# Performance work log

Hardware: AMD Instinct MI355X
Metric: run time of the kernel (lower is better)

The kernel has to match this reference:

```python
import jax, jax.numpy as jnp
import numpy as np

HEADS = 16
NEG_INF = -1e30


def rel_shift(t):
    # t: [b, h, i, j] with i == j; Transformer-XL style relative shift
    b, h, i, j = t.shape
    t = jnp.pad(t, ((0, 0), (0, 0), (0, 0), (1, 0)))  # zero pad on last dim front
    t = t.reshape(b, h, j + 1, i)[:, :, 1:]
    return t.reshape(b, h, i, j)


def setup_inputs() -> dict:
    key = jax.random.key(0)
    ks = jax.random.split(key, 8)
    b, n, dim = 2, 2048, 1024
    d_head = dim // HEADS
    w = 0.02
    return {
        "x": jax.random.normal(ks[0], (b, n, dim), dtype=jnp.float32),
        "pos_emb": jax.random.normal(ks[1], (n, dim), dtype=jnp.float32),
        "Wq": jax.random.normal(ks[2], (dim, dim), dtype=jnp.float32) * w,
        "bq": jnp.zeros((dim,), dtype=jnp.float32),
        "Wkv": jax.random.normal(ks[3], (dim, 2 * dim), dtype=jnp.float32) * w,
        "bkv": jnp.zeros((2 * dim,), dtype=jnp.float32),
        "Wp": jax.random.normal(ks[4], (dim, d_head), dtype=jnp.float32) * w,
        "bp": jnp.zeros((d_head,), dtype=jnp.float32),
        "Wo": jax.random.normal(ks[5], (dim, dim), dtype=jnp.float32) * w,
        "bo": jnp.zeros((dim,), dtype=jnp.float32),
    }


def reference(x, pos_emb, Wq, bq, Wkv, bkv, Wp, bp, Wo, bo):
    b, n, dim = x.shape
    h = HEADS
    d = dim // h
    scale = d ** -0.5

    q = (x @ Wq + bq).reshape(b, n, h, d).transpose(0, 2, 1, 3)  # b h n d
    kv = x @ Wkv + bkv
    k, v = jnp.split(kv, 2, axis=-1)
    k = k.reshape(b, n, h, d).transpose(0, 2, 1, 3)
    v = v.reshape(b, n, h, d).transpose(0, 2, 1, 3)

    dots = jnp.einsum('bhid,bhjd->bhij', q, k) * scale

    # relative position bias
    p = pos_emb @ Wp + bp  # [n, d]
    pos_attn = jnp.einsum('bhid,jd->bhij', q, p) * scale
    dots = dots + rel_shift(pos_attn)

    # causal mask
    causal = jnp.triu(jnp.ones((n, n), dtype=bool), 1)
    dots = jnp.where(causal[None, None], NEG_INF, dots)

    attn = jax.nn.softmax(dots, axis=-1)
    out = jnp.einsum('bhij,bhjd->bhid', attn, v)
    out = out.transpose(0, 2, 1, 3).reshape(b, n, dim)
    return out @ Wo + bo
```

## Files before the change

kernel.cpp:

```cpp
#include <hip/hip_runtime.h>
#include <hip/hip_bf16.h>
#include <cstdint>
#include <cstddef>

#define SEQ_N 2048
#define DIM   1024
#define NHEAD 16
#define DH    64

typedef __bf16 bf16;
typedef __attribute__((ext_vector_type(8))) __bf16 bf16x8;
typedef __attribute__((ext_vector_type(4))) __bf16 bf16x4;
typedef __attribute__((ext_vector_type(4))) float f32x4;

__device__ __forceinline__ void gl_lds16(const bf16* g, bf16* l) {
    __builtin_amdgcn_global_load_lds(
        (const __attribute__((address_space(1))) unsigned int*)g,
        (__attribute__((address_space(3))) unsigned int*)l, 16, 0, 0);
}

__global__ __launch_bounds__(256) void prep_kernel(
    const float* __restrict__ x, const float* __restrict__ pos,
    const float* __restrict__ Wq, const float* __restrict__ Wkv,
    const float* __restrict__ Wo, const float* __restrict__ Wp,
    bf16* __restrict__ xb, bf16* __restrict__ posb,
    bf16* __restrict__ WqkvT, bf16* __restrict__ WoT, bf16* __restrict__ WpT)
{
    int bid = blockIdx.x;
    if (bid < 6144) {
        const int NX = 4096 * 1024;
        int i = (bid * 256 + threadIdx.x) * 4;
        if (i < NX) {
            float4 v = *(const float4*)&x[i];
            xb[i + 0] = (bf16)v.x; xb[i + 1] = (bf16)v.y;
            xb[i + 2] = (bf16)v.z; xb[i + 3] = (bf16)v.w;
        } else {
            int j = i - NX;
            float4 v = *(const float4*)&pos[j];
            posb[j + 0] = (bf16)v.x; posb[j + 1] = (bf16)v.y;
            posb[j + 2] = (bf16)v.z; posb[j + 3] = (bf16)v.w;
        }
        return;
    }
    __shared__ float t[32][33];
    bid -= 6144;
    const float* src; bf16* dst; int tidx, nx, N;
    if (bid < 1024)      { src = Wq;  dst = WqkvT;                       tidx = bid;        nx = 32; N = 1024; }
    else if (bid < 3072) { src = Wkv; dst = WqkvT + (size_t)1024 * 1024; tidx = bid - 1024; nx = 64; N = 2048; }
    else if (bid < 4096) { src = Wo;  dst = WoT;                         tidx = bid - 3072; nx = 32; N = 1024; }
    else                 { src = Wp;  dst = WpT;                         tidx = bid - 4096; nx = 2;  N = 64;   }
    int n0 = (tidx % nx) * 32, k0 = (tidx / nx) * 32;
    int tx = threadIdx.x & 31, ty = threadIdx.x >> 5;
    #pragma unroll
    for (int r = ty; r < 32; r += 8)
        t[r][tx] = src[(size_t)(k0 + r) * N + n0 + tx];
    __syncthreads();
    #pragma unroll
    for (int r = ty; r < 32; r += 8)
        dst[(size_t)(n0 + r) * 1024 + k0 + tx] = (bf16)t[tx][r];
}

__global__ __launch_bounds__(256) void qkvp_kernel(
    const bf16* __restrict__ xb, const bf16* __restrict__ WqkvT,
    const bf16* __restrict__ posb, const bf16* __restrict__ WpT,
    const float* __restrict__ bq, const float* __restrict__ bkv,
    const float* __restrict__ bp,
    bf16* __restrict__ qbuf, bf16* __restrict__ kbuf,
    bf16* __restrict__ vtbuf, bf16* __restrict__ pfrag)
{
    __shared__ __align__(16) bf16 sm[128 * 132];
    bf16* At = sm;
    bf16* Bt = sm + 128 * 64;
    const int tid = threadIdx.x, w = tid >> 6, lane = tid & 63;
    const int q = lane >> 4, ln15 = lane & 15;
    const int lr = lane >> 3, c_log = (lane & 7) ^ lr;
    const int bx = blockIdx.x, by = blockIdx.y;
    const int m0 = by * 128;

    if (bx == 24) {
        if (by >= 16) return;
        f32x4 acc[2][4] = {};
        for (int k0 = 0; k0 < 1024; k0 += 64) {
            __syncthreads();
            #pragma unroll
            for (int t = 0; t < 4; ++t)
                gl_lds16(&posb[(size_t)(m0 + 32 * w + 8 * t + lr) * 1024 + k0 + c_log * 8],
                         &At[(32 * w + 8 * t) * 64]);
            #pragma unroll
            for (int t = 0; t < 2; ++t)
                gl_lds16(&WpT[(size_t)(16 * w + 8 * t + lr) * 1024 + k0 + c_log * 8],
                         &Bt[(16 * w + 8 * t) * 64]);
            __syncthreads();
            bf16x8 bfr[2][4];
            #pragma unroll
            for (int ks = 0; ks < 2; ++ks)
                #pragma unroll
                for (int sn = 0; sn < 4; ++sn) {
                    int rb = 16 * sn + ln15;
                    bfr[ks][sn] = *(const bf16x8*)&Bt[(rb * 8 + ((4 * ks + q) ^ (rb & 7))) * 8];
                }
            #pragma unroll
            for (int sm2 = 0; sm2 < 2; ++sm2) {
                int ra = 32 * w + 16 * sm2 + ln15;
                #pragma unroll
                for (int ks = 0; ks < 2; ++ks) {
                    bf16x8 af = *(const bf16x8*)&At[(ra * 8 + ((4 * ks + q) ^ (ra & 7))) * 8];
                    #pragma unroll
                    for (int sn = 0; sn < 4; ++sn)
                        acc[sm2][sn] = __builtin_amdgcn_mfma_f32_16x16x32_bf16(
                            af, bfr[ks][sn], acc[sm2][sn], 0, 0, 0);
                }
            }
        }
        #pragma unroll
        for (int sm2 = 0; sm2 < 2; ++sm2)
            #pragma unroll
            for (int sn = 0; sn < 4; ++sn)
                #pragma unroll
                for (int r = 0; r < 4; ++r) {
                    int row = m0 + 32 * w + 16 * sm2 + 4 * q + r;
                    int d = 16 * sn + ln15;
                    int sb = row >> 4, lnp = row & 15;
                    int ks2 = d >> 5, qd = (d >> 3) & 3, e = d & 7;
                    pfrag[(((size_t)sb * 2 + ks2) * 64 + qd * 16 + lnp) * 8 + e] =
                        (bf16)(acc[sm2][sn][r] + bp[d]);
                }
        return;
    }

    const int n0 = bx * 128;
    const int wm = w >> 1, wn = w & 1;
    f32x4 acc[4][4] = {};

    for (int k0 = 0; k0 < 1024; k0 += 64) {
        __syncthreads();
        #pragma unroll
        for (int t = 0; t < 4; ++t) {
            int r = 32 * w + 8 * t + lr;
            gl_lds16(&xb[(size_t)(m0 + r) * 1024 + k0 + c_log * 8],
                     &At[(32 * w + 8 * t) * 64]);
            gl_lds16(&WqkvT[(size_t)(n0 + r) * 1024 + k0 + c_log * 8],
                     &Bt[(32 * w + 8 * t) * 64]);
        }
        __syncthreads();

        bf16x8 af[2][4], bfr[2][4];
        #pragma unroll
        for (int ks = 0; ks < 2; ++ks)
            #pragma unroll
            for (int s = 0; s < 4; ++s) {
                int ra = 64 * wm + 16 * s + ln15;
                af[ks][s]  = *(const bf16x8*)&At[(ra * 8 + ((4 * ks + q) ^ (ra & 7))) * 8];
                int rb = 64 * wn + 16 * s + ln15;
                bfr[ks][s] = *(const bf16x8*)&Bt[(rb * 8 + ((4 * ks + q) ^ (rb & 7))) * 8];
            }
        #pragma unroll
        for (int ks = 0; ks < 2; ++ks)
            #pragma unroll
            for (int si = 0; si < 4; ++si)
                #pragma unroll
                for (int sj = 0; sj < 4; ++sj)
                    acc[si][sj] = __builtin_amdgcn_mfma_f32_16x16x32_bf16(
                        af[ks][si], bfr[ks][sj], acc[si][sj], 0, 0, 0);
    }

    if (bx < 16) {
        const float QSCL = 0.125f * 1.44269504088896341f;
        #pragma unroll
        for (int si = 0; si < 4; ++si)
            #pragma unroll
            for (int sj = 0; sj < 4; ++sj)
                #pragma unroll
                for (int r = 0; r < 4; ++r) {
                    int row = m0 + 64 * wm + 16 * si + 4 * q + r;
                    int col = n0 + 64 * wn + 16 * sj + ln15;
                    float v = acc[si][sj][r] + (col < 1024 ? bq[col] : bkv[col - 1024]);
                    if (col < 1024) qbuf[(size_t)row * 1024 + col] = (bf16)(v * QSCL);
                    else            kbuf[(size_t)row * 1024 + (col - 1024)] = (bf16)v;
                }
    } else {
        __syncthreads();
        #pragma unroll
        for (int si = 0; si < 4; ++si)
            #pragma unroll
            for (int sj = 0; sj < 4; ++sj) {
                int dL = 64 * wn + 16 * sj + ln15;
                int tL = 64 * wm + 16 * si + 4 * q;
                float bias = bkv[1024 + (bx - 16) * 128 + dL];
                bf16x4 o4;
                #pragma unroll
                for (int r = 0; r < 4; ++r)
                    o4[r] = (bf16)(acc[si][sj][r] + bias);
                *(bf16x4*)&sm[dL * 132 + tL] = o4;
            }
        __syncthreads();
        const int b = m0 >> 11;
        const int t0 = m0 & 2047;
        const int h0 = (bx - 16) * 2;
        #pragma unroll
        for (int p = 0; p < 16; ++p) {
            int d = (tid >> 5) + 8 * p;
            int t = (tid & 31) * 4;
            bf16x4 v4 = *(const bf16x4*)&sm[d * 132 + t];
            int rowv = (b * NHEAD + h0 + (d >> 6)) * DH + (d & 63);
            *(bf16x4*)&vtbuf[(size_t)rowv * SEQ_N + t0 + t] = v4;
        }
    }
}

__global__ __launch_bounds__(256, 4) void attn_mfma_kernel(
    const bf16* __restrict__ qb,
    const bf16* __restrict__ kb,
    const bf16* __restrict__ vt,
    const bf16* __restrict__ pfrag,
    bf16* __restrict__ ob,
    float* __restrict__ Opart,
    float2* __restrict__ MLpart)
{
    const int f   = (int)blockIdx.x;
    const int xcd = f & 7;
    const int jj  = f >> 3;
    const int c   = jj & 31;
    const int rr  = jj >> 5;
    const int bh  = xcd * 4 + (c & 3);
    const int g   = c >> 2;
    int qblk, lo, hi, part;
    switch (rr) {
        case 0:  qblk = 16 + 2 * g; lo = 0;  hi = 16;       part = 0;  break;
        case 1:  qblk = 17 + 2 * g; lo = 0;  hi = 16;       part = 0;  break;
        case 2:  qblk = 31 - g;     lo = 16; hi = qblk + 1; part = 1;  break;
        case 3:  qblk = 16 + g;     lo = 16; hi = qblk + 1; part = 1;  break;
        case 4:  qblk = 15 - g;     lo = 0;  hi = qblk + 1; part = -1; break;
        default: qblk = g;          lo = 0;  hi = qblk + 1; part = -1; break;
    }
    const int bi = bh >> 4, hh = bh & 15;
    const int i0 = qblk << 6;
    const int tid = threadIdx.x, w = tid >> 6, lane = tid & 63;
    const int q = lane >> 4, ln15 = lane & 15;
    const int lr = lane >> 3, c_log = (lane & 7) ^ lr;

    __shared__ __align__(16) bf16 smem[13568];
    bf16* S2L = smem + w * 1344;
    bf16* Pw  = smem + w * 1344;
    bf16* Ks  = smem + 5376;
    bf16* Vs  = smem + 9472;

    const bf16* qbase = qb + ((size_t)(bi * SEQ_N + i0)) * DIM + hh * DH;
    const bf16* kbase = kb + ((size_t)bi * SEQ_N) * DIM + hh * DH;
    const bf16* vbase = vt + ((size_t)(bi * NHEAD + hh) * DH) * SEQ_N;

    bf16x8 qf0 = *(const bf16x8*)&qbase[(size_t)(16 * w + ln15) * DIM + q * 8];
    bf16x8 qf1 = *(const bf16x8*)&qbase[(size_t)(16 * w + ln15) * DIM + 32 + q * 8];

    const int A0 = 127 - 4 * qblk - w;
    f32x4 s2r4;
    {
        int sb0 = A0 + 4 * lo;
        bf16x8 f0 = *(const bf16x8*)&pfrag[(((size_t)sb0 * 2 + 0) * 64 + lane) * 8];
        bf16x8 f1 = *(const bf16x8*)&pfrag[(((size_t)sb0 * 2 + 1) * 64 + lane) * 8];
        f32x4 a = {0.f, 0.f, 0.f, 0.f};
        a = __builtin_amdgcn_mfma_f32_16x16x32_bf16(f0, qf0, a, 0, 0, 0);
        a = __builtin_amdgcn_mfma_f32_16x16x32_bf16(f1, qf1, a, 0, 0, 0);
        s2r4 = a;
    }

    float m_run = -1e30f, l_run = 0.f;
    f32x4 O_T[4] = {};

    for (int jt = lo; jt < hi; ++jt) {
        const int j0 = jt << 6;

        bf16x8 pfA[4][2];
        #pragma unroll
        for (int ss = 1; ss <= 4; ++ss) {
            int sb = A0 + 4 * jt + ss;
            if (sb > 127) sb = 127;
            pfA[ss-1][0] = *(const bf16x8*)&pfrag[(((size_t)sb * 2 + 0) * 64 + lane) * 8];
            pfA[ss-1][1] = *(const bf16x8*)&pfrag[(((size_t)sb * 2 + 1) * 64 + lane) * 8];
        }
        #pragma unroll
        for (int t = 0; t < 2; ++t) {
            int r = 16 * w + 8 * t + lr;
            gl_lds16(kbase + (size_t)(j0 + r) * DIM + c_log * 8,
                     &Ks[(16 * w + 8 * t) * 64]);
            gl_lds16(vbase + (size_t)r * SEQ_N + j0 + c_log * 8,
                     &Vs[(16 * w + 8 * t) * 64]);
        }

        {
            f32x4 s2r[5];
            s2r[0] = s2r4;
            #pragma unroll
            for (int ss = 1; ss <= 4; ++ss) {
                f32x4 a = {0.f, 0.f, 0.f, 0.f};
                a = __builtin_amdgcn_mfma_f32_16x16x32_bf16(pfA[ss-1][0], qf0, a, 0, 0, 0);
                a = __builtin_amdgcn_mfma_f32_16x16x32_bf16(pfA[ss-1][1], qf1, a, 0, 0, 0);
                s2r[ss] = a;
            }
            s2r4 = s2r[4];
            #pragma unroll
            for (int ss = 0; ss < 5; ++ss) {
                bf16x4 v4;
                #pragma unroll
                for (int r = 0; r < 4; ++r)
                    v4[r] = (bf16)s2r[ss][r];
                *(bf16x4*)&S2L[ln15 * 84 + 16 * ss + 4 * q] = v4;
            }
        }

        __syncthreads();

        float sv[4][4];
        __builtin_amdgcn_s_setprio(1);
        #pragma unroll
        for (int sn = 0; sn < 4; ++sn) {
            int rk = 16 * sn + ln15;
            bf16x8 k0f = *(const bf16x8*)&Ks[(rk * 8 + ((q    ) ^ (rk & 7))) * 8];
            bf16x8 k1f = *(const bf16x8*)&Ks[(rk * 8 + ((4 + q) ^ (rk & 7))) * 8];
            f32x4 a;
            #pragma unroll
            for (int r = 0; r < 4; ++r)
                a[r] = (float)S2L[ln15 * 84 + 15 - ln15 + 16 * sn + 4 * q + r];
            a = __builtin_amdgcn_mfma_f32_16x16x32_bf16(k0f, qf0, a, 0, 0, 0);
            a = __builtin_amdgcn_mfma_f32_16x16x32_bf16(k1f, qf1, a, 0, 0, 0);
            #pragma unroll
            for (int r = 0; r < 4; ++r)
                sv[sn][r] = a[r];
        }
        __builtin_amdgcn_s_setprio(0);
        if (jt == qblk) {
            #pragma unroll
            for (int sn = 0; sn < 4; ++sn)
                #pragma unroll
                for (int r = 0; r < 4; ++r)
                    if (16 * sn + 4 * q + r > 16 * w + ln15)
                        sv[sn][r] = -1e30f;
        }

        float mx = sv[0][0];
        #pragma unroll
        for (int sn = 0; sn < 4; ++sn)
            #pragma unroll
            for (int r = 0; r < 4; ++r)
                mx = fmaxf(mx, sv[sn][r]);
        mx = fmaxf(mx, __shfl_xor(mx, 16));
        mx = fmaxf(mx, __shfl_xor(mx, 32));
        const float mn = fmaxf(m_run, mx);
        float sum = 0.f;
        #pragma unroll
        for (int sn = 0; sn < 4; ++sn)
            #pragma unroll
            for (int r = 0; r < 4; ++r) {
                float e = exp2f(sv[sn][r] - mn);
                sv[sn][r] = e;
                sum += e;
            }
        sum += __shfl_xor(sum, 16);
        sum += __shfl_xor(sum, 32);
        if (__all(mx <= m_run)) {
            l_run += sum;
        } else {
            const float alpha = exp2f(m_run - mn);
            l_run = l_run * alpha + sum;
            #pragma unroll
            for (int sd = 0; sd < 4; ++sd)
                #pragma unroll
                for (int r = 0; r < 4; ++r)
                    O_T[sd][r] *= alpha;
        }
        m_run = mn;

        #pragma unroll
        for (int sn = 0; sn < 4; ++sn) {
            int chunk = (2 * sn + (q >> 1)) ^ (ln15 & 7);
            bf16x4 v4;
            #pragma unroll
            for (int r = 0; r < 4; ++r)
                v4[r] = (bf16)sv[sn][r];
            *(bf16x4*)&Pw[ln15 * 64 + chunk * 8 + 4 * (q & 1)] = v4;
        }

        __builtin_amdgcn_s_waitcnt(0);

        __builtin_amdgcn_s_setprio(1);
        #pragma unroll
        for (int ks = 0; ks < 2; ++ks) {
            bf16x8 pT = *(const bf16x8*)&Pw[ln15 * 64 + (((4 * ks + q) ^ (ln15 & 7))) * 8];
            #pragma unroll
            for (int sd = 0; sd < 4; ++sd) {
                int rv = 16 * sd + ln15;
                bf16x8 vf = *(const bf16x8*)&Vs[(rv * 8 + ((4 * ks + q) ^ (rv & 7))) * 8];
                O_T[sd] = __builtin_amdgcn_mfma_f32_16x16x32_bf16(vf, pT, O_T[sd], 0, 0, 0);
            }
        }
        __builtin_amdgcn_s_setprio(0);
        __syncthreads();
    }

    const int row = 16 * w + ln15;
    if (part < 0) {
        const float inv = 1.0f / l_run;
        const size_t grow = (size_t)bi * SEQ_N + i0 + row;
        #pragma unroll
        for (int sd = 0; sd < 4; ++sd) {
            bf16x4 o4;
            #pragma unroll
            for (int r = 0; r < 4; ++r)
                o4[r] = (bf16)(O_T[sd][r] * inv);
            *(bf16x4*)&ob[grow * DIM + hh * DH + 16 * sd + 4 * q] = o4;
        }
    } else {
        const int slot = (bh * 16 + (qblk - 16)) * 2 + part;
        float* op = Opart + (size_t)slot * 4096 + row * 64;
        #pragma unroll
        for (int sd = 0; sd < 4; ++sd)
            *(f32x4*)&op[16 * sd + 4 * q] = O_T[sd];
        if (lane < 16)
            MLpart[slot * 64 + row] = make_float2(m_run, l_run);
    }
}

__global__ __launch_bounds__(256) void merge_kernel(
    const float* __restrict__ Opart, const float2* __restrict__ MLpart,
    bf16* __restrict__ ob)
{
    const int pb = blockIdx.x;
    const int bh = pb >> 4, qblk = 16 + (pb & 15);
    const int bi = bh >> 4, hh = bh & 15;
    const int row = threadIdx.x >> 2;
    const int d0 = (threadIdx.x & 3) * 16;

    float2 ml0 = MLpart[(pb * 2 + 0) * 64 + row];
    float2 ml1 = MLpart[(pb * 2 + 1) * 64 + row];
    float m = fmaxf(ml0.x, ml1.x);
    float a0 = exp2f(ml0.x - m), a1 = exp2f(ml1.x - m);
    float inv = 1.0f / (ml0.y * a0 + ml1.y * a1);

    const float* o0 = Opart + ((size_t)(pb * 2 + 0)) * 4096 + row * 64 + d0;
    const float* o1 = Opart + ((size_t)(pb * 2 + 1)) * 4096 + row * 64 + d0;
    bf16* dst = ob + ((size_t)(bi * SEQ_N + qblk * 64 + row)) * DIM + hh * DH + d0;
    #pragma unroll
    for (int k = 0; k < 4; ++k) {
        float4 v0 = *(const float4*)&o0[4 * k];
        float4 v1 = *(const float4*)&o1[4 * k];
        bf16x4 o4;
        o4[0] = (bf16)((v0.x * a0 + v1.x * a1) * inv);
        o4[1] = (bf16)((v0.y * a0 + v1.y * a1) * inv);
        o4[2] = (bf16)((v0.z * a0 + v1.z * a1) * inv);
        o4[3] = (bf16)((v0.w * a0 + v1.w * a1) * inv);
        *(bf16x4*)&dst[4 * k] = o4;
    }
}

__global__ __launch_bounds__(256) void outproj_kernel(
    const bf16* __restrict__ ab, const bf16* __restrict__ WoT,
    const float* __restrict__ bo, float* __restrict__ out)
{
    __shared__ __align__(16) bf16 At[128 * 64];
    __shared__ __align__(16) bf16 Bt[64 * 64];
    const int tid = threadIdx.x, w = tid >> 6, lane = tid & 63;
    const int q = lane >> 4, ln15 = lane & 15;
    const int lr = lane >> 3, c_log = (lane & 7) ^ lr;
    const int m0 = blockIdx.y * 128, n0 = blockIdx.x * 64;

    f32x4 acc[2][4] = {};
    for (int k0 = 0; k0 < 1024; k0 += 64) {
        __syncthreads();
        #pragma unroll
        for (int t = 0; t < 4; ++t)
            gl_lds16(&ab[(size_t)(m0 + 32 * w + 8 * t + lr) * 1024 + k0 + c_log * 8],
                     &At[(32 * w + 8 * t) * 64]);
        #pragma unroll
        for (int t = 0; t < 2; ++t)
            gl_lds16(&WoT[(size_t)(n0 + 16 * w + 8 * t + lr) * 1024 + k0 + c_log * 8],
                     &Bt[(16 * w + 8 * t) * 64]);
        __syncthreads();

        bf16x8 bfr[2][4];
        #pragma unroll
        for (int ks = 0; ks < 2; ++ks)
            #pragma unroll
            for (int sn = 0; sn < 4; ++sn) {
                int rb = 16 * sn + ln15;
                bfr[ks][sn] = *(const bf16x8*)&Bt[(rb * 8 + ((4 * ks + q) ^ (rb & 7))) * 8];
            }
        #pragma unroll
        for (int sm2 = 0; sm2 < 2; ++sm2) {
            int ra = 32 * w + 16 * sm2 + ln15;
            #pragma unroll
            for (int ks = 0; ks < 2; ++ks) {
                bf16x8 af = *(const bf16x8*)&At[(ra * 8 + ((4 * ks + q) ^ (ra & 7))) * 8];
                #pragma unroll
                for (int sn = 0; sn < 4; ++sn)
                    acc[sm2][sn] = __builtin_amdgcn_mfma_f32_16x16x32_bf16(
                        af, bfr[ks][sn], acc[sm2][sn], 0, 0, 0);
            }
        }
    }
    #pragma unroll
    for (int sm2 = 0; sm2 < 2; ++sm2)
        #pragma unroll
        for (int sn = 0; sn < 4; ++sn) {
            int col = n0 + 16 * sn + ln15;
            float bias = bo[col];
            #pragma unroll
            for (int r = 0; r < 4; ++r) {
                int row = m0 + 32 * w + 16 * sm2 + 4 * q + r;
                out[(size_t)row * 1024 + col] = acc[sm2][sn][r] + bias;
            }
        }
}

extern "C" void kernel_launch(void* const* d_in, const int* in_sizes, int n_in,
                              void* d_out, int out_size, void* d_ws, size_t ws_size,
                              hipStream_t stream)
{
    const float* x    = (const float*)d_in[0];
    const float* pos  = (const float*)d_in[1];
    const float* Wq   = (const float*)d_in[2];
    const float* bq   = (const float*)d_in[3];
    const float* Wkv  = (const float*)d_in[4];
    const float* bkv  = (const float*)d_in[5];
    const float* Wp   = (const float*)d_in[6];
    const float* bp   = (const float*)d_in[7];
    const float* Wo   = (const float*)d_in[8];
    const float* bo   = (const float*)d_in[9];
    float* out = (float*)d_out;

    const int M = 2 * SEQ_N;
    char* ws = (char*)d_ws;
    bf16* xb     = (bf16*)ws;  ws += (size_t)M * DIM * 2;
    bf16* posb   = (bf16*)ws;  ws += (size_t)SEQ_N * DIM * 2;
    bf16* WqkvT  = (bf16*)ws;  ws += (size_t)3072 * 1024 * 2;
    bf16* WoT    = (bf16*)ws;  ws += (size_t)DIM * DIM * 2;
    bf16* WpT    = (bf16*)ws;  ws += (size_t)DH * DIM * 2;
    bf16* qbuf   = (bf16*)ws;  ws += (size_t)M * DIM * 2;
    bf16* kbuf   = (bf16*)ws;  ws += (size_t)M * DIM * 2;
    bf16* vtbuf  = (bf16*)ws;  ws += (size_t)M * DIM * 2;
    bf16* pfrag  = (bf16*)ws;  ws += (size_t)512 * 1024;
    bf16* abuf   = (bf16*)ws;

    float*  Opart  = (float*)d_ws;
    float2* MLpart = (float2*)((char*)d_ws + (size_t)1024 * 4096 * 4);

    dim3 blk(256);
    prep_kernel<<<dim3(10304), blk, 0, stream>>>(
        x, pos, Wq, Wkv, Wo, Wp, xb, posb, WqkvT, WoT, WpT);

    qkvp_kernel<<<dim3(25, 32), blk, 0, stream>>>(
        xb, WqkvT, posb, WpT, bq, bkv, bp, qbuf, kbuf, vtbuf, pfrag);

    attn_mfma_kernel<<<dim3(1536), blk, 0, stream>>>(
        qbuf, kbuf, vtbuf, pfrag, abuf, Opart, MLpart);

    merge_kernel<<<dim3(512), blk, 0, stream>>>(Opart, MLpart, abuf);

    outproj_kernel<<<dim3(16, 32), blk, 0, stream>>>(
        abuf, WoT, bo, out);
}
```

Before: 246.6 us.

## Widen attention key tile from 64 to 128 columns per iteration

The attention loop now processes 128 key/value positions per iteration instead of 64, which halves the number of loop trips, barriers and softmax rescale steps. LDS buffers for K, V, the shifted position bias and P are enlarged and relaid out to match, and the causal mask is applied on the last tile when a diagonal block is present. The cost is nearly double the LDS footprint and more registers per thread, which may lower occupancy under the 4-waves launch bound. When the tile straddles the diagonal, half of it can be fully masked work.

```diff
diff --git a/kernel.cpp b/kernel.cpp
--- a/kernel.cpp
+++ b/kernel.cpp
@@ -224,26 +224,30 @@
     const int rr  = jj >> 5;
     const int bh  = xcd * 4 + (c & 3);
     const int g   = c >> 2;
-    int qblk, lo, hi, part;
+    int qblk, lo64, hi64, part;
     switch (rr) {
-        case 0:  qblk = 16 + 2 * g; lo = 0;  hi = 16;       part = 0;  break;
-        case 1:  qblk = 17 + 2 * g; lo = 0;  hi = 16;       part = 0;  break;
-        case 2:  qblk = 31 - g;     lo = 16; hi = qblk + 1; part = 1;  break;
-        case 3:  qblk = 16 + g;     lo = 16; hi = qblk + 1; part = 1;  break;
-        case 4:  qblk = 15 - g;     lo = 0;  hi = qblk + 1; part = -1; break;
-        default: qblk = g;          lo = 0;  hi = qblk + 1; part = -1; break;
-    }
+        case 0:  qblk = 16 + 2 * g; lo64 = 0;  hi64 = 16;       part = 0;  break;
+        case 1:  qblk = 17 + 2 * g; lo64 = 0;  hi64 = 16;       part = 0;  break;
+        case 2:  qblk = 31 - g;     lo64 = 16; hi64 = qblk + 1; part = 1;  break;
+        case 3:  qblk = 16 + g;     lo64 = 16; hi64 = qblk + 1; part = 1;  break;
+        case 4:  qblk = 15 - g;     lo64 = 0;  hi64 = qblk + 1; part = -1; break;
+        default: qblk = g;          lo64 = 0;  hi64 = qblk + 1; part = -1; break;
+    }
+    const int lo = lo64 >> 1;
+    const int hi = (hi64 + 1) >> 1;
     const int bi = bh >> 4, hh = bh & 15;
     const int i0 = qblk << 6;
     const int tid = threadIdx.x, w = tid >> 6, lane = tid & 63;
     const int q = lane >> 4, ln15 = lane & 15;
     const int lr = lane >> 3, c_log = (lane & 7) ^ lr;
-
-    __shared__ __align__(16) bf16 smem[13568];
-    bf16* S2L = smem + w * 1344;
-    bf16* Pw  = smem + w * 1344;
-    bf16* Ks  = smem + 5376;
-    bf16* Vs  = smem + 9472;
+    const bool hasDiag = (part != 0);
+    const int moff = ((qblk & 1) << 6) + 16 * w + ln15;
+
+    __shared__ __align__(16) bf16 smem[25856];
+    bf16* S2L = smem + w * 2368;
+    bf16* Pw  = smem + w * 2368;
+    bf16* Ks  = smem + 9472;
+    bf16* Vs  = smem + 17664;
 
     const bf16* qbase = qb + ((size_t)(bi * SEQ_N + i0)) * DIM + hh * DH;
     const bf16* kbase = kb + ((size_t)bi * SEQ_N) * DIM + hh * DH;
@@ -255,7 +259,7 @@
     const int A0 = 127 - 4 * qblk - w;
     f32x4 s2r4;
     {
-        int sb0 = A0 + 4 * lo;
+        int sb0 = A0 + 8 * lo;
         bf16x8 f0 = *(const bf16x8*)&pfrag[(((size_t)sb0 * 2 + 0) * 64 + lane) * 8];
         bf16x8 f1 = *(const bf16x8*)&pfrag[(((size_t)sb0 * 2 + 1) * 64 + lane) * 8];
         f32x4 a = {0.f, 0.f, 0.f, 0.f};
@@ -268,59 +272,56 @@
     f32x4 O_T[4] = {};
 
     for (int jt = lo; jt < hi; ++jt) {
-        const int j0 = jt << 6;
-
-        bf16x8 pfA[4][2];
-        #pragma unroll
-        for (int ss = 1; ss <= 4; ++ss) {
-            int sb = A0 + 4 * jt + ss;
-            if (sb > 127) sb = 127;
-            pfA[ss-1][0] = *(const bf16x8*)&pfrag[(((size_t)sb * 2 + 0) * 64 + lane) * 8];
-            pfA[ss-1][1] = *(const bf16x8*)&pfrag[(((size_t)sb * 2 + 1) * 64 + lane) * 8];
-        }
-        #pragma unroll
-        for (int t = 0; t < 2; ++t) {
-            int r = 16 * w + 8 * t + lr;
-            gl_lds16(kbase + (size_t)(j0 + r) * DIM + c_log * 8,
-                     &Ks[(16 * w + 8 * t) * 64]);
-            gl_lds16(vbase + (size_t)r * SEQ_N + j0 + c_log * 8,
-                     &Vs[(16 * w + 8 * t) * 64]);
+        const int j0 = jt << 7;
+
+        #pragma unroll
+        for (int t = 0; t < 4; ++t)
+            gl_lds16(kbase + (size_t)(j0 + 32 * w + 8 * t + lr) * DIM + c_log * 8,
+                     &Ks[(32 * w + 8 * t) * 64]);
+        #pragma unroll
+        for (int t = 0; t < 4; ++t) {
+            int rv_ = 16 * w + 4 * t + (lane >> 4);
+            int cs  = (lane & 15) ^ (rv_ & 7);
+            gl_lds16(vbase + (size_t)rv_ * SEQ_N + j0 + cs * 8,
+                     &Vs[(16 * w + 4 * t) * 128]);
         }
 
         {
-            f32x4 s2r[5];
-            s2r[0] = s2r4;
-            #pragma unroll
-            for (int ss = 1; ss <= 4; ++ss) {
+            bf16x4 v4;
+            #pragma unroll
+            for (int r = 0; r < 4; ++r)
+                v4[r] = (bf16)s2r4[r];
+            *(bf16x4*)&S2L[ln15 * 148 + 4 * q] = v4;
+            #pragma unroll
+            for (int ss = 1; ss <= 8; ++ss) {
+                int sb = A0 + 8 * jt + ss;
+                if (sb > 127) sb = 127;
+                bf16x8 f0 = *(const bf16x8*)&pfrag[(((size_t)sb * 2 + 0) * 64 + lane) * 8];
+                bf16x8 f1 = *(const bf16x8*)&pfrag[(((size_t)sb * 2 + 1) * 64 + lane) * 8];
                 f32x4 a = {0.f, 0.f, 0.f, 0.f};
-                a = __builtin_amdgcn_mfma_f32_16x16x32_bf16(pfA[ss-1][0], qf0, a, 0, 0, 0);
-                a = __builtin_amdgcn_mfma_f32_16x16x32_bf16(pfA[ss-1][1], qf1, a, 0, 0, 0);
-                s2r[ss] = a;
-            }
-            s2r4 = s2r[4];
-            #pragma unroll
-            for (int ss = 0; ss < 5; ++ss) {
-                bf16x4 v4;
+                a = __builtin_amdgcn_mfma_f32_16x16x32_bf16(f0, qf0, a, 0, 0, 0);
+                a = __builtin_amdgcn_mfma_f32_16x16x32_bf16(f1, qf1, a, 0, 0, 0);
                 #pragma unroll
                 for (int r = 0; r < 4; ++r)
-                    v4[r] = (bf16)s2r[ss][r];
-                *(bf16x4*)&S2L[ln15 * 84 + 16 * ss + 4 * q] = v4;
-            }
-        }
-
-        __syncthreads();
-
-        float sv[4][4];
+                    v4[r] = (bf16)a[r];
+                *(bf16x4*)&S2L[ln15 * 148 + 16 * ss + 4 * q] = v4;
+                if (ss == 8) s2r4 = a;
+            }
+        }
+
+        __syncthreads();
+
+        float sv[8][4];
         __builtin_amdgcn_s_setprio(1);
         #pragma unroll
-        for (int sn = 0; sn < 4; ++sn) {
+        for (int sn = 0; sn < 8; ++sn) {
             int rk = 16 * sn + ln15;
             bf16x8 k0f = *(const bf16x8*)&Ks[(rk * 8 + ((q    ) ^ (rk & 7))) * 8];
             bf16x8 k1f = *(const bf16x8*)&Ks[(rk * 8 + ((4 + q) ^ (rk & 7))) * 8];
             f32x4 a;
             #pragma unroll
             for (int r = 0; r < 4; ++r)
-                a[r] = (float)S2L[ln15 * 84 + 15 - ln15 + 16 * sn + 4 * q + r];
+                a[r] = (float)S2L[ln15 * 148 + 15 - ln15 + 16 * sn + 4 * q + r];
             a = __builtin_amdgcn_mfma_f32_16x16x32_bf16(k0f, qf0, a, 0, 0, 0);
             a = __builtin_amdgcn_mfma_f32_16x16x32_bf16(k1f, qf1, a, 0, 0, 0);
             #pragma unroll
@@ -328,18 +329,18 @@
                 sv[sn][r] = a[r];
         }
         __builtin_amdgcn_s_setprio(0);
-        if (jt == qblk) {
-            #pragma unroll
-            for (int sn = 0; sn < 4; ++sn)
+        if (hasDiag && jt == hi - 1) {
+            #pragma unroll
+            for (int sn = 0; sn < 8; ++sn)
                 #pragma unroll
                 for (int r = 0; r < 4; ++r)
-                    if (16 * sn + 4 * q + r > 16 * w + ln15)
+                    if (16 * sn + 4 * q + r > moff)
                         sv[sn][r] = -1e30f;
         }
 
         float mx = sv[0][0];
         #pragma unroll
-        for (int sn = 0; sn < 4; ++sn)
+        for (int sn = 0; sn < 8; ++sn)
             #pragma unroll
             for (int r = 0; r < 4; ++r)
                 mx = fmaxf(mx, sv[sn][r]);
@@ -348,7 +349,7 @@
         const float mn = fmaxf(m_run, mx);
         float sum = 0.f;
         #pragma unroll
-        for (int sn = 0; sn < 4; ++sn)
+        for (int sn = 0; sn < 8; ++sn)
             #pragma unroll
             for (int r = 0; r < 4; ++r) {
                 float e = exp2f(sv[sn][r] - mn);
@@ -371,25 +372,25 @@
         m_run = mn;
 
         #pragma unroll
-        for (int sn = 0; sn < 4; ++sn) {
+        for (int sn = 0; sn < 8; ++sn) {
             int chunk = (2 * sn + (q >> 1)) ^ (ln15 & 7);
             bf16x4 v4;
             #pragma unroll
             for (int r = 0; r < 4; ++r)
                 v4[r] = (bf16)sv[sn][r];
-            *(bf16x4*)&Pw[ln15 * 64 + chunk * 8 + 4 * (q & 1)] = v4;
+            *(bf16x4*)&Pw[ln15 * 128 + chunk * 8 + 4 * (q & 1)] = v4;
         }
 
         __builtin_amdgcn_s_waitcnt(0);
 
         __builtin_amdgcn_s_setprio(1);
         #pragma unroll
-        for (int ks = 0; ks < 2; ++ks) {
-            bf16x8 pT = *(const bf16x8*)&Pw[ln15 * 64 + (((4 * ks + q) ^ (ln15 & 7))) * 8];
+        for (int ks = 0; ks < 4; ++ks) {
+            bf16x8 pT = *(const bf16x8*)&Pw[ln15 * 128 + (((4 * ks + q) ^ (ln15 & 7))) * 8];
             #pragma unroll
             for (int sd = 0; sd < 4; ++sd) {
                 int rv = 16 * sd + ln15;
-                bf16x8 vf = *(const bf16x8*)&Vs[(rv * 8 + ((4 * ks + q) ^ (rv & 7))) * 8];
+                bf16x8 vf = *(const bf16x8*)&Vs[rv * 128 + (((4 * ks + q) ^ (rv & 7))) * 8];
                 O_T[sd] = __builtin_amdgcn_mfma_f32_16x16x32_bf16(vf, pT, O_T[sd], 0, 0, 0);
             }
         }
```

Measured after the change: 258.2 us. +4.7%, slower.
